# Optimization experiments

Measured on AMD Instinct MI355X. Metric: run time of the kernel, lower is better.

The kernel has to match this reference:

```python
import jax, jax.numpy as jnp
import numpy as np

N_NODES = 50000
N_EDGES = 600000
DIN, DH, DOUT = 128, 256, 128
BN_EPS = 1e-5
LRELU_SLOPE = 0.01


def setup_inputs() -> dict:
    key = jax.random.key(0)
    ks = jax.random.split(key, 16)
    rn = lambda k, s, sc=0.05: jax.random.normal(k, s, dtype=jnp.float32) * sc
    return {
        'nodes': jax.random.normal(ks[0], (N_NODES, DIN), dtype=jnp.float32),
        'src': jax.random.randint(ks[1], (N_EDGES,), 0, N_NODES, dtype=jnp.int32),
        'dst': jax.random.randint(ks[2], (N_EDGES,), 0, N_NODES, dtype=jnp.int32),
        # FeedForward params
        'Wf1': rn(ks[3], (DIN, DH)), 'bf1': jnp.zeros((DH,), jnp.float32),
        'gf1': jnp.ones((DH,), jnp.float32), 'bef1': jnp.zeros((DH,), jnp.float32),
        'Wf2': rn(ks[4], (DH, DIN)), 'bf2': jnp.zeros((DIN,), jnp.float32),
        'gf2': jnp.ones((DIN,), jnp.float32), 'bef2': jnp.zeros((DIN,), jnp.float32),
        # SAGEConv 1 (in->hidden)
        'Ws1': rn(ks[5], (DIN, DH)), 'Wn1': rn(ks[6], (DIN, DH)), 'b1': jnp.zeros((DH,), jnp.float32),
        'gs1': jnp.ones((DH,), jnp.float32), 'bs1': jnp.zeros((DH,), jnp.float32),
        # SAGEConv 2 (hidden->out)
        'Ws2': rn(ks[7], (DH, DOUT)), 'Wn2': rn(ks[8], (DH, DOUT)), 'b2': jnp.zeros((DOUT,), jnp.float32),
        'gs2': jnp.ones((DOUT,), jnp.float32), 'bs2': jnp.zeros((DOUT,), jnp.float32),
    }


def _bn(x, gamma, beta):
    # BatchNorm1d, training mode: batch stats over node dim, biased variance
    mu = jnp.mean(x, axis=0)
    var = jnp.mean(jnp.square(x - mu), axis=0)
    return (x - mu) * jax.lax.rsqrt(var + BN_EPS) * gamma + beta


def _sage_mean(x, src, dst, Wself, Wneigh, bias):
    # DGL SAGEConv('mean'): out = x@Wself + mean_{src->dst}(x[src])@Wneigh + bias
    n = x.shape[0]
    deg = jax.ops.segment_sum(jnp.ones_like(src, dtype=x.dtype), dst, num_segments=n)
    agg = jax.ops.segment_sum(x[src], dst, num_segments=n)  # [N, d] irregular scatter-add
    h_neigh = agg / jnp.maximum(deg, 1.0)[:, None]
    return x @ Wself + h_neigh @ Wneigh + bias


def reference(nodes, src, dst, Wf1, bf1, gf1, bef1, Wf2, bf2, gf2, bef2,
              Ws1, Wn1, b1, gs1, bs1, Ws2, Wn2, b2, gs2, bs2):
    # FeedForward (dropout=0 -> identity)
    h = jax.nn.relu(_bn(nodes @ Wf1 + bf1, gf1, bef1))
    h = jax.nn.relu(_bn(h @ Wf2 + bf2, gf2, bef2))
    # SAGE layer 1
    h1 = _sage_mean(h, src, dst, Ws1, Wn1, b1)
    h1 = jax.nn.leaky_relu(_bn(h1, gs1, bs1), LRELU_SLOPE)
    # SAGE layer 2
    h2 = _sage_mean(h1, src, dst, Ws2, Wn2, b2)
    return jax.nn.leaky_relu(_bn(h2, gs2, bs2), LRELU_SLOPE)
```

## Files before the change

### kernel.cpp

```cpp
#include <hip/hip_runtime.h>

#define DIN 128
#define BN_EPS 1e-5f

typedef __attribute__((ext_vector_type(8))) short bf16x8;
typedef __attribute__((ext_vector_type(8))) unsigned short us8;
typedef __attribute__((ext_vector_type(4))) float f32x4;

__device__ __forceinline__ ushort f2bf(float f) {
    unsigned u = __float_as_uint(f);
    u += 0x7fffu + ((u >> 16) & 1u);
    return (ushort)(u >> 16);
}
__device__ __forceinline__ float bf2f(ushort h) {
    return __uint_as_float(((unsigned)h) << 16);
}

template<int KC, int NT, int STATS>
__global__ __launch_bounds__(256) void gemm_wreg(
    const ushort* __restrict__ A, const ushort* __restrict__ BT,
    ushort* __restrict__ C, int mStrips, int N, int K, int logNG,
    float* __restrict__ gsums, float* __restrict__ gsqs)
{
    int tid = threadIdx.x;
    int lane = tid & 63;
    int gw = blockIdx.x * 4 + (tid >> 6);
    int wg = gw & ((1 << logNG) - 1);
    int set = gw >> logNG;
    int totalSets = (gridDim.x * 4) >> logNG;
    int cl = lane & 15, q = lane >> 4;
    int colBase = wg * (16 * NT);

    bf16x8 bf[NT][KC];
    #pragma unroll
    for (int nt = 0; nt < NT; nt++) {
        const ushort* bp = BT + (long)(colBase + nt * 16 + cl) * K + q * 8;
        #pragma unroll
        for (int kc = 0; kc < KC; kc++)
            bf[nt][kc] = *(const bf16x8*)(bp + kc * 32);
    }

    float ssum[NT];
    float ssq[NT];
    #pragma unroll
    for (int nt = 0; nt < NT; nt++) { ssum[nt] = 0.f; ssq[nt] = 0.f; }

    for (int strip = set; strip < mStrips; strip += totalSets) {
        int rowBase = strip * 16;
        const ushort* ap = A + (long)(rowBase + cl) * K + q * 8;
        bf16x8 af[KC];
        #pragma unroll
        for (int kc = 0; kc < KC; kc++)
            af[kc] = *(const bf16x8*)(ap + kc * 32);
        f32x4 acc[NT] = {};
        #pragma unroll
        for (int kc = 0; kc < KC; kc++)
            #pragma unroll
            for (int nt = 0; nt < NT; nt++)
                acc[nt] = __builtin_amdgcn_mfma_f32_16x16x32_bf16(af[kc], bf[nt][kc], acc[nt], 0, 0, 0);
        #pragma unroll
        for (int nt = 0; nt < NT; nt++) {
            #pragma unroll
            for (int r = 0; r < 4; r++) {
                float v = acc[nt][r];
                long row = rowBase + q * 4 + r;
                C[row * N + colBase + nt * 16 + cl] = f2bf(v);
                if (STATS) { ssum[nt] += v; ssq[nt] += v * v; }
            }
        }
    }

    if (STATS) {
        #pragma unroll
        for (int nt = 0; nt < NT; nt++) {
            ssum[nt] += __shfl_xor(ssum[nt], 16, 64);
            ssum[nt] += __shfl_xor(ssum[nt], 32, 64);
            ssq[nt]  += __shfl_xor(ssq[nt], 16, 64);
            ssq[nt]  += __shfl_xor(ssq[nt], 32, 64);
        }
        if (q == 0) {
            #pragma unroll
            for (int nt = 0; nt < NT; nt++) {
                atomicAdd(&gsums[colBase + nt * 16 + cl], ssum[nt]);
                atomicAdd(&gsqs[colBase + nt * 16 + cl], ssq[nt]);
            }
        }
    }
}

__global__ __launch_bounds__(256) void setup_all(
    const float* __restrict__ nodes, ushort* __restrict__ Xbf, int nConv4, int nbConv,
    const float* __restrict__ W0, const float* __restrict__ W1,
    const float* __restrict__ W2, const float* __restrict__ W3,
    const float* __restrict__ W4, const float* __restrict__ W5,
    ushort* __restrict__ WT,
    int* __restrict__ zeroInts, int nZero4, int nbZero,
    float* __restrict__ stats)
{
    int b = blockIdx.x;
    int tid = threadIdx.x;
    if (b < nbConv) {
        int t = b * 256 + tid;
        if (t < nConv4) {
            float4 v = *(const float4*)&nodes[(long)t * 4];
            ushort4 o; o.x = f2bf(v.x); o.y = f2bf(v.y); o.z = f2bf(v.z); o.w = f2bf(v.w);
            *(ushort4*)&Xbf[(long)t * 4] = o;
        }
        return;
    }
    b -= nbConv;
    if (b < 768) {
        int seg = b >> 7;
        const float* W; int logK, dstBase, stride, kOff;
        switch (seg) {
            case 0: W = W0; logK = 7; dstBase = 0;      stride = 128; kOff = 0;   break;
            case 1: W = W1; logK = 8; dstBase = 32768;  stride = 256; kOff = 0;   break;
            case 2: W = W2; logK = 7; dstBase = 65536;  stride = 256; kOff = 0;   break;
            case 3: W = W3; logK = 7; dstBase = 65536;  stride = 256; kOff = 128; break;
            case 4: W = W4; logK = 8; dstBase = 131072; stride = 256; kOff = 0;   break;
            default:W = W5; logK = 8; dstBase = 163840; stride = 256; kOff = 0;   break;
        }
        int t = (b & 127) * 256 + tid;
        int N = 32768 >> logK;
        int k = t & ((1 << logK) - 1);
        int n = t >> logK;
        WT[(long)dstBase + (long)n * stride + kOff + k] = f2bf(W[(long)k * N + n]);
        return;
    }
    b -= 768;
    if (b < nbZero) {
        int t = b * 256 + tid;
        if (t < nZero4) *(int4*)&zeroInts[(long)t * 4] = make_int4(0, 0, 0, 0);
        return;
    }
    b -= nbZero;
    int t = b * 256 + tid;
    if (t < 512) *(float4*)&stats[(long)t * 4] = make_float4(0, 0, 0, 0);
}

template<int LOGN>
__global__ __launch_bounds__(256) void bnact_bf16(
    const ushort* __restrict__ X,
    const float* __restrict__ sums, const float* __restrict__ sqs,
    const float* __restrict__ gamma, const float* __restrict__ beta, float invM,
    ushort* __restrict__ O, int nRows, int outStride, float negSlope)
{
    constexpr int NCH = 1 << LOGN;
    __shared__ float ssc[NCH], ssh[NCH];
    int tid = threadIdx.x;
    if (tid < NCH) {
        float mean = sums[tid] * invM;
        float var = sqs[tid] * invM - mean * mean;
        float sc = gamma[tid] * rsqrtf(var + BN_EPS);
        ssc[tid] = sc;
        ssh[tid] = beta[tid] - mean * sc;
    }
    __syncthreads();
    int cb = (tid * 8) & (NCH - 1);
    float4 sA = *(const float4*)&ssc[cb];
    float4 sB = *(const float4*)&ssc[cb + 4];
    float4 hA = *(const float4*)&ssh[cb];
    float4 hB = *(const float4*)&ssh[cb + 4];
    const int rpb = (256 * 8) >> LOGN;
    int r0 = blockIdx.x * rpb + ((tid * 8) >> LOGN);
    int rstride = gridDim.x * rpb;
    for (int row = r0; row < nRows; row += rstride) {
        us8 v = *(const us8*)&X[(long)row * NCH + cb];
        float f0 = bf2f(v[0]) * sA.x + hA.x; f0 = (f0 > 0.f) ? f0 : f0 * negSlope;
        float f1 = bf2f(v[1]) * sA.y + hA.y; f1 = (f1 > 0.f) ? f1 : f1 * negSlope;
        float f2 = bf2f(v[2]) * sA.z + hA.z; f2 = (f2 > 0.f) ? f2 : f2 * negSlope;
        float f3 = bf2f(v[3]) * sA.w + hA.w; f3 = (f3 > 0.f) ? f3 : f3 * negSlope;
        float f4 = bf2f(v[4]) * sB.x + hB.x; f4 = (f4 > 0.f) ? f4 : f4 * negSlope;
        float f5 = bf2f(v[5]) * sB.y + hB.y; f5 = (f5 > 0.f) ? f5 : f5 * negSlope;
        float f6 = bf2f(v[6]) * sB.z + hB.z; f6 = (f6 > 0.f) ? f6 : f6 * negSlope;
        float f7 = bf2f(v[7]) * sB.w + hB.w; f7 = (f7 > 0.f) ? f7 : f7 * negSlope;
        us8 o;
        o[0] = f2bf(f0); o[1] = f2bf(f1); o[2] = f2bf(f2); o[3] = f2bf(f3);
        o[4] = f2bf(f4); o[5] = f2bf(f5); o[6] = f2bf(f6); o[7] = f2bf(f7);
        *(us8*)&O[(long)row * outStride + cb] = o;
    }
}

__global__ __launch_bounds__(256) void bnact_f32(
    float* __restrict__ X,
    const float* __restrict__ sums, const float* __restrict__ sqs,
    const float* __restrict__ gamma, const float* __restrict__ beta, float invM,
    int nRows, float negSlope)
{
    __shared__ float ssc[128], ssh[128];
    int tid = threadIdx.x;
    if (tid < 128) {
        float mean = sums[tid] * invM;
        float var = sqs[tid] * invM - mean * mean;
        float sc = gamma[tid] * rsqrtf(var + BN_EPS);
        ssc[tid] = sc;
        ssh[tid] = beta[tid] - mean * sc;
    }
    __syncthreads();
    int cb = (tid * 4) & 127;
    float4 sc = *(const float4*)&ssc[cb];
    float4 sh = *(const float4*)&ssh[cb];
    int r0 = blockIdx.x * 8 + ((tid * 4) >> 7);
    int rstride = gridDim.x * 8;
    for (int row = r0; row < nRows; row += rstride) {
        float4 v = *(const float4*)&X[(long)row * 128 + cb];
        float a = v.x * sc.x + sh.x; a = (a > 0.f) ? a : a * negSlope;
        float b = v.y * sc.y + sh.y; b = (b > 0.f) ? b : b * negSlope;
        float d = v.z * sc.z + sh.z; d = (d > 0.f) ? d : d * negSlope;
        float e = v.w * sc.w + sh.w; e = (e > 0.f) ? e : e * negSlope;
        *(float4*)&X[(long)row * 128 + cb] = make_float4(a, b, d, e);
    }
}

__global__ __launch_bounds__(256) void colstats128(
    const float* __restrict__ X, float* __restrict__ sums, float* __restrict__ sqs, int M)
{
    __shared__ float ss[128], sq[128];
    int tid = threadIdx.x;
    if (tid < 128) { ss[tid] = 0.f; sq[tid] = 0.f; }
    __syncthreads();
    int cg = tid & 31;
    int worker = (blockIdx.x << 3) | (tid >> 5);
    int totalW = gridDim.x << 3;
    float4 s4 = make_float4(0, 0, 0, 0), q4 = make_float4(0, 0, 0, 0);
    for (int r = worker; r < M; r += totalW) {
        float4 v = *(const float4*)&X[(long)r * 128 + cg * 4];
        s4.x += v.x; s4.y += v.y; s4.z += v.z; s4.w += v.w;
        q4.x += v.x * v.x; q4.y += v.y * v.y; q4.z += v.z * v.z; q4.w += v.w * v.w;
    }
    atomicAdd(&ss[cg * 4 + 0], s4.x); atomicAdd(&sq[cg * 4 + 0], q4.x);
    atomicAdd(&ss[cg * 4 + 1], s4.y); atomicAdd(&sq[cg * 4 + 1], q4.y);
    atomicAdd(&ss[cg * 4 + 2], s4.z); atomicAdd(&sq[cg * 4 + 2], q4.z);
    atomicAdd(&ss[cg * 4 + 3], s4.w); atomicAdd(&sq[cg * 4 + 3], q4.w);
    __syncthreads();
    if (tid < 128) { atomicAdd(&sums[tid], ss[tid]); atomicAdd(&sqs[tid], sq[tid]); }
}

__global__ void degcount_kernel(const int* __restrict__ dst, int* __restrict__ degi, int E)
{
    int i = blockIdx.x * blockDim.x + threadIdx.x;
    if (i < E) atomicAdd(&degi[dst[i]], 1);
}

__global__ __launch_bounds__(256) void scan_block_sums(const int* __restrict__ degi,
                                                       int* __restrict__ partial, int n)
{
    __shared__ int s[256];
    int i = blockIdx.x * 256 + threadIdx.x;
    s[threadIdx.x] = (i < n) ? degi[i] : 0;
    __syncthreads();
    for (int off = 128; off > 0; off >>= 1) {
        if (threadIdx.x < off) s[threadIdx.x] += s[threadIdx.x + off];
        __syncthreads();
    }
    if (threadIdx.x == 0) partial[blockIdx.x] = s[0];
}

__global__ __launch_bounds__(256) void scan_final(const int* __restrict__ degi,
                                                  const int* __restrict__ partial,
                                                  int* __restrict__ rowstart, int n, int nb)
{
    __shared__ int s[256];
    __shared__ int ps[256];
    int tid = threadIdx.x;
    ps[tid] = (tid < nb && tid < (int)blockIdx.x) ? partial[tid] : 0;
    __syncthreads();
    for (int off = 128; off > 0; off >>= 1) {
        if (tid < off) ps[tid] += ps[tid + off];
        __syncthreads();
    }
    int offset = ps[0];
    int i = blockIdx.x * 256 + tid;
    int v = (i < n) ? degi[i] : 0;
    s[tid] = v;
    __syncthreads();
    for (int off = 1; off < 256; off <<= 1) {
        int t = (tid >= off) ? s[tid - off] : 0;
        __syncthreads();
        s[tid] += t;
        __syncthreads();
    }
    if (i < n) rowstart[i] = offset + s[tid] - v;
}

__global__ void fillcsr_kernel(const int* __restrict__ src, const int* __restrict__ dst,
                               const int* __restrict__ rowstart, int* __restrict__ cursor,
                               int* __restrict__ csr, int E)
{
    int i = blockIdx.x * blockDim.x + threadIdx.x;
    if (i < E) {
        int d = dst[i];
        int p = atomicAdd(&cursor[d], 1);
        csr[rowstart[d] + p] = src[i];
    }
}

__device__ __forceinline__ void acc8(float acc[8], us8 v) {
    #pragma unroll
    for (int e = 0; e < 8; e++) acc[e] += bf2f(v[e]);
}

__global__ __launch_bounds__(256) void gather16_bf(
    const ushort* __restrict__ X, const int* __restrict__ rowstart,
    const int* __restrict__ degi, const int* __restrict__ csr,
    ushort* __restrict__ O, int nN)
{
    int wv = (blockIdx.x * blockDim.x + threadIdx.x) >> 6;
    int lane = threadIdx.x & 63;
    if (wv >= nN) return;
    int g = lane >> 4;
    int sc = lane & 15;
    int start = rowstart[wv], d = degi[wv];
    const ushort* Xc = X + sc * 8;
    float acc[8] = {};
    if (d > 0) {
        int dm = (d < 64) ? d : 64;
        int idx_l = csr[start + ((lane < dm) ? lane : (dm - 1))];
        int j = 0;
        for (; j + 8 <= dm; j += 8) {
            int i0 = __shfl(idx_l, j + g, 64);
            int i1 = __shfl(idx_l, j + 4 + g, 64);
            us8 v0 = *(const us8*)(Xc + (long)i0 * 256);
            us8 v1 = *(const us8*)(Xc + (long)i1 * 256);
            acc8(acc, v0);
            acc8(acc, v1);
        }
        if (j + 4 <= dm) {
            int i0 = __shfl(idx_l, j + g, 64);
            us8 v0 = *(const us8*)(Xc + (long)i0 * 256);
            acc8(acc, v0);
            j += 4;
        }
        int rem = dm - j;
        if (rem > 0) {
            int sl = j + ((g < rem) ? g : (rem - 1));
            int i0 = __shfl(idx_l, sl, 64);
            if (g < rem) {
                us8 v0 = *(const us8*)(Xc + (long)i0 * 256);
                acc8(acc, v0);
            }
        }
        for (int jj = 64; jj < d; jj += 4) {
            if (jj + g < d) {
                int i0 = csr[start + jj + g];
                us8 v0 = *(const us8*)(Xc + (long)i0 * 256);
                acc8(acc, v0);
            }
        }
    }
    #pragma unroll
    for (int e = 0; e < 8; e++) {
        acc[e] += __shfl_xor(acc[e], 16, 64);
        acc[e] += __shfl_xor(acc[e], 32, 64);
    }
    if (g == 0) {
        float inv = 1.f / fmaxf((float)d, 1.f);
        us8 o;
        #pragma unroll
        for (int e = 0; e < 8; e++) o[e] = f2bf(acc[e] * inv);
        *(us8*)(O + (long)wv * 256 + sc * 8) = o;
    }
}

__global__ __launch_bounds__(256) void gather16_fuse(
    const ushort* __restrict__ Z, const int* __restrict__ rowstart,
    const int* __restrict__ degi, const int* __restrict__ csr,
    float* __restrict__ O, int nN)
{
    int wv = (blockIdx.x * blockDim.x + threadIdx.x) >> 6;
    int lane = threadIdx.x & 63;
    if (wv >= nN) return;
    int g = lane >> 4;
    int sc = lane & 15;
    int start = rowstart[wv], d = degi[wv];
    const ushort* Zc = Z + sc * 8;
    us8 selfv = *(const us8*)(Zc + (long)wv * 256 + 128);
    float acc[8] = {};
    if (d > 0) {
        int dm = (d < 64) ? d : 64;
        int idx_l = csr[start + ((lane < dm) ? lane : (dm - 1))];
        int j = 0;
        for (; j + 8 <= dm; j += 8) {
            int i0 = __shfl(idx_l, j + g, 64);
            int i1 = __shfl(idx_l, j + 4 + g, 64);
            us8 v0 = *(const us8*)(Zc + (long)i0 * 256);
            us8 v1 = *(const us8*)(Zc + (long)i1 * 256);
            acc8(acc, v0);
            acc8(acc, v1);
        }
        if (j + 4 <= dm) {
            int i0 = __shfl(idx_l, j + g, 64);
            us8 v0 = *(const us8*)(Zc + (long)i0 * 256);
            acc8(acc, v0);
            j += 4;
        }
        int rem = dm - j;
        if (rem > 0) {
            int sl = j + ((g < rem) ? g : (rem - 1));
            int i0 = __shfl(idx_l, sl, 64);
            if (g < rem) {
                us8 v0 = *(const us8*)(Zc + (long)i0 * 256);
                acc8(acc, v0);
            }
        }
        for (int jj = 64; jj < d; jj += 4) {
            if (jj + g < d) {
                int i0 = csr[start + jj + g];
                us8 v0 = *(const us8*)(Zc + (long)i0 * 256);
                acc8(acc, v0);
            }
        }
    }
    #pragma unroll
    for (int e = 0; e < 8; e++) {
        acc[e] += __shfl_xor(acc[e], 16, 64);
        acc[e] += __shfl_xor(acc[e], 32, 64);
    }
    if (g == 0) {
        float inv = 1.f / fmaxf((float)d, 1.f);
        float r[8];
        #pragma unroll
        for (int e = 0; e < 8; e++) r[e] = acc[e] * inv + bf2f(selfv[e]);
        float* op = O + (long)wv * 128 + sc * 8;
        *(float4*)op = make_float4(r[0], r[1], r[2], r[3]);
        *(float4*)(op + 4) = make_float4(r[4], r[5], r[6], r[7]);
    }
}

extern "C" void kernel_launch(void* const* d_in, const int* in_sizes, int n_in,
                              void* d_out, int out_size, void* d_ws, size_t ws_size,
                              hipStream_t stream)
{
    const float* nodes = (const float*)d_in[0];
    const int*   src   = (const int*)d_in[1];
    const int*   dst   = (const int*)d_in[2];
    const float* Wf1   = (const float*)d_in[3];
    const float* gf1   = (const float*)d_in[5];
    const float* bef1  = (const float*)d_in[6];
    const float* Wf2   = (const float*)d_in[7];
    const float* gf2   = (const float*)d_in[9];
    const float* bef2  = (const float*)d_in[10];
    const float* Ws1   = (const float*)d_in[11];
    const float* Wn1   = (const float*)d_in[12];
    const float* gs1   = (const float*)d_in[14];
    const float* bs1   = (const float*)d_in[15];
    const float* Ws2   = (const float*)d_in[16];
    const float* Wn2   = (const float*)d_in[17];
    const float* gs2   = (const float*)d_in[19];
    const float* bs2   = (const float*)d_in[20];

    int nN = in_sizes[0] / DIN;
    int nE = in_sizes[1];
    float* out = (float*)d_out;
    int mStrips = nN / 16;
    float invM = 1.0f / nN;

    ushort* PRE = (ushort*)d_ws;
    ushort* BF1 = PRE + (size_t)nN * 256;
    ushort* BF2 = BF1 + (size_t)nN * 256;
    float* stats = (float*)(BF2 + (size_t)nN * 256);
    float* scale = stats + 2048;
    float* shift = scale + 256;
    ushort* WT   = (ushort*)(shift + 256);
    int* degi     = (int*)(WT + 196608);
    int* cursor   = degi + nN;
    int* rowstart = cursor + nN;
    int* partial  = rowstart + nN;
    int* csr      = partial + 256;

    ushort* Wf1T = WT;
    ushort* Wf2T = WT + 32768;
    ushort* Wc1T = WT + 65536;
    ushort* Wc2T = WT + 131072;

    dim3 blk(256);
    auto cdiv = [](int a, int b) { return (a + b - 1) / b; };
    int nScanBlocks = cdiv(nN, 256);

    int nConv4 = nN * DIN / 4;
    int nbConv = cdiv(nConv4, 256);
    int nZero4 = (2 * nN) / 4;
    int nbZero = cdiv(nZero4, 256);
    setup_all<<<dim3(nbConv + 768 + nbZero + 2), blk, 0, stream>>>(
        nodes, BF1, nConv4, nbConv,
        Wf1, Wf2, Ws1, Wn1, Wn2, Ws2, WT,
        degi, nZero4, nbZero, stats);

    degcount_kernel<<<dim3(cdiv(nE, 256)), blk, 0, stream>>>(dst, degi, nE);
    scan_block_sums<<<dim3(nScanBlocks), blk, 0, stream>>>(degi, partial, nN);
    scan_final<<<dim3(nScanBlocks), blk, 0, stream>>>(degi, partial, rowstart, nN, nScanBlocks);
    fillcsr_kernel<<<dim3(cdiv(nE, 256)), blk, 0, stream>>>(src, dst, rowstart, cursor, csr, nE);

    gemm_wreg<4, 4, 1><<<dim3(512), blk, 0, stream>>>(BF1, Wf1T, PRE, mStrips, 256, 128, 2, stats, stats + 256);
    bnact_bf16<8><<<dim3(2048), blk, 0, stream>>>(PRE, stats, stats + 256, gf1, bef1, invM,
                                                  BF1, nN, 256, 0.0f);

    gemm_wreg<8, 2, 1><<<dim3(512), blk, 0, stream>>>(BF1, Wf2T, PRE, mStrips, 128, 256, 2, stats + 512, stats + 768);
    bnact_bf16<7><<<dim3(2048), blk, 0, stream>>>(PRE, stats + 512, stats + 768, gf2, bef2, invM,
                                                  BF2, nN, 256, 0.0f);

    gather16_bf<<<dim3(cdiv(nN * 64, 256)), blk, 0, stream>>>(BF2, rowstart, degi, csr, BF2 + 128, nN);

    gemm_wreg<8, 2, 1><<<dim3(1024), blk, 0, stream>>>(BF2, Wc1T, PRE, mStrips, 256, 256, 3, stats + 1024, stats + 1280);
    bnact_bf16<8><<<dim3(2048), blk, 0, stream>>>(PRE, stats + 1024, stats + 1280, gs1, bs1, invM,
                                                  BF1, nN, 256, 0.01f);

    gemm_wreg<8, 2, 0><<<dim3(1024), blk, 0, stream>>>(BF1, Wc2T, BF2, mStrips, 256, 256, 3, nullptr, nullptr);
    gather16_fuse<<<dim3(cdiv(nN * 64, 256)), blk, 0, stream>>>(BF2, rowstart, degi, csr, out, nN);

    colstats128<<<dim3(120), blk, 0, stream>>>(out, stats + 1536, stats + 1792, nN);
    bnact_f32<<<dim3(2048), blk, 0, stream>>>(out, stats + 1536, stats + 1792, gs2, bs2, invM,
                                              nN, 0.01f);
}
```

Measured before the change: 406.9 us.

## Stage A strips in swizzled LDS shared across waves with register prefetch

The weight-stationary GEMM used to have each wave load its own copy of each A strip from global memory. Now all four waves in a block cover different column groups of the same 16-row strip. The strip is loaded cooperatively into XOR-swizzled shared memory, and the next strip is prefetched into registers while the current one is computed. This cuts redundant global reads of A and overlaps loads with MFMA work, at the cost of two block barriers per strip and more registers for the larger NT=4 tiles in the SAGE GEMMs.

```diff
diff --git a/kernel.cpp b/kernel.cpp
--- a/kernel.cpp
+++ b/kernel.cpp
@@ -17,19 +17,23 @@
 }
 
 template<int KC, int NT, int STATS>
-__global__ __launch_bounds__(256) void gemm_wreg(
+__global__ __launch_bounds__(256) void gemm_lds(
     const ushort* __restrict__ A, const ushort* __restrict__ BT,
-    ushort* __restrict__ C, int mStrips, int N, int K, int logNG,
+    ushort* __restrict__ C, int mStrips, int N,
     float* __restrict__ gsums, float* __restrict__ gsqs)
 {
+    constexpr int K = KC * 32;
+    constexpr int CPR = KC * 4;
+    constexpr int LOGCPR = (KC == 4) ? 4 : 5;
+    constexpr int LPL = KC / 4;
+    __shared__ ushort abuf[16 * K];
+
     int tid = threadIdx.x;
     int lane = tid & 63;
-    int gw = blockIdx.x * 4 + (tid >> 6);
-    int wg = gw & ((1 << logNG) - 1);
-    int set = gw >> logNG;
-    int totalSets = (gridDim.x * 4) >> logNG;
+    int w = tid >> 6;
     int cl = lane & 15, q = lane >> 4;
-    int colBase = wg * (16 * NT);
+    int colBase = w * (16 * NT);
+    int chBase = w * (16 * KC);
 
     bf16x8 bf[NT][KC];
     #pragma unroll
@@ -40,24 +44,49 @@
             bf[nt][kc] = *(const bf16x8*)(bp + kc * 32);
     }
 
-    float ssum[NT];
-    float ssq[NT];
+    float ssum[NT], ssq[NT];
     #pragma unroll
     for (int nt = 0; nt < NT; nt++) { ssum[nt] = 0.f; ssq[nt] = 0.f; }
 
-    for (int strip = set; strip < mStrips; strip += totalSets) {
-        int rowBase = strip * 16;
-        const ushort* ap = A + (long)(rowBase + cl) * K + q * 8;
+    int totalSets = gridDim.x;
+    int s0 = blockIdx.x;
+
+    us8 stg[LPL];
+    {
+        const ushort* As = A + (long)s0 * 16 * K;
+        #pragma unroll
+        for (int u = 0; u < LPL; u++)
+            stg[u] = *(const us8*)(As + (chBase + u * 64 + lane) * 8);
+        #pragma unroll
+        for (int u = 0; u < LPL; u++) {
+            int ch = chBase + u * 64 + lane;
+            int r = ch >> LOGCPR;
+            int c = ch & (CPR - 1);
+            *(us8*)(abuf + (((r << LOGCPR) + (c ^ (r & 7))) * 8)) = stg[u];
+        }
+    }
+    __syncthreads();
+
+    for (int s = s0; s < mStrips; s += totalSets) {
+        int nxt = s + totalSets;
+        bool more = nxt < mStrips;
+        if (more) {
+            const ushort* As = A + (long)nxt * 16 * K;
+            #pragma unroll
+            for (int u = 0; u < LPL; u++)
+                stg[u] = *(const us8*)(As + (chBase + u * 64 + lane) * 8);
+        }
         bf16x8 af[KC];
         #pragma unroll
         for (int kc = 0; kc < KC; kc++)
-            af[kc] = *(const bf16x8*)(ap + kc * 32);
+            af[kc] = *(const bf16x8*)(abuf + (((cl << LOGCPR) + ((kc * 4 + q) ^ (cl & 7))) * 8));
         f32x4 acc[NT] = {};
         #pragma unroll
         for (int kc = 0; kc < KC; kc++)
             #pragma unroll
             for (int nt = 0; nt < NT; nt++)
                 acc[nt] = __builtin_amdgcn_mfma_f32_16x16x32_bf16(af[kc], bf[nt][kc], acc[nt], 0, 0, 0);
+        int rowBase = s * 16;
         #pragma unroll
         for (int nt = 0; nt < NT; nt++) {
             #pragma unroll
@@ -68,6 +97,17 @@
                 if (STATS) { ssum[nt] += v; ssq[nt] += v * v; }
             }
         }
+        __syncthreads();
+        if (more) {
+            #pragma unroll
+            for (int u = 0; u < LPL; u++) {
+                int ch = chBase + u * 64 + lane;
+                int r = ch >> LOGCPR;
+                int c = ch & (CPR - 1);
+                *(us8*)(abuf + (((r << LOGCPR) + (c ^ (r & 7))) * 8)) = stg[u];
+            }
+        }
+        __syncthreads();
     }
 
     if (STATS) {
@@ -491,21 +531,21 @@
     scan_final<<<dim3(nScanBlocks), blk, 0, stream>>>(degi, partial, rowstart, nN, nScanBlocks);
     fillcsr_kernel<<<dim3(cdiv(nE, 256)), blk, 0, stream>>>(src, dst, rowstart, cursor, csr, nE);
 
-    gemm_wreg<4, 4, 1><<<dim3(512), blk, 0, stream>>>(BF1, Wf1T, PRE, mStrips, 256, 128, 2, stats, stats + 256);
+    gemm_lds<4, 4, 1><<<dim3(512), blk, 0, stream>>>(BF1, Wf1T, PRE, mStrips, 256, stats, stats + 256);
     bnact_bf16<8><<<dim3(2048), blk, 0, stream>>>(PRE, stats, stats + 256, gf1, bef1, invM,
                                                   BF1, nN, 256, 0.0f);
 
-    gemm_wreg<8, 2, 1><<<dim3(512), blk, 0, stream>>>(BF1, Wf2T, PRE, mStrips, 128, 256, 2, stats + 512, stats + 768);
+    gemm_lds<8, 2, 1><<<dim3(512), blk, 0, stream>>>(BF1, Wf2T, PRE, mStrips, 128, stats + 512, stats + 768);
     bnact_bf16<7><<<dim3(2048), blk, 0, stream>>>(PRE, stats + 512, stats + 768, gf2, bef2, invM,
                                                   BF2, nN, 256, 0.0f);
 
     gather16_bf<<<dim3(cdiv(nN * 64, 256)), blk, 0, stream>>>(BF2, rowstart, degi, csr, BF2 + 128, nN);
 
-    gemm_wreg<8, 2, 1><<<dim3(1024), blk, 0, stream>>>(BF2, Wc1T, PRE, mStrips, 256, 256, 3, stats + 1024, stats + 1280);
+    gemm_lds<8, 4, 1><<<dim3(512), blk, 0, stream>>>(BF2, Wc1T, PRE, mStrips, 256, stats + 1024, stats + 1280);
     bnact_bf16<8><<<dim3(2048), blk, 0, stream>>>(PRE, stats + 1024, stats + 1280, gs1, bs1, invM,
                                                   BF1, nN, 256, 0.01f);
 
-    gemm_wreg<8, 2, 0><<<dim3(1024), blk, 0, stream>>>(BF1, Wc2T, BF2, mStrips, 256, 256, 3, nullptr, nullptr);
+    gemm_lds<8, 4, 0><<<dim3(512), blk, 0, stream>>>(BF1, Wc2T, BF2, mStrips, 256, nullptr, nullptr);
     gather16_fuse<<<dim3(cdiv(nN * 64, 256)), blk, 0, stream>>>(BF2, rowstart, degi, csr, out, nN);
 
     colstats128<<<dim3(120), blk, 0, stream>>>(out, stats + 1536, stats + 1792, nN);
```

Result: faster. 372.3 us (-8.5%).
